# Performance work log

Hardware: AMD Instinct MI355X
Metric: run time of the kernel (lower is better)

## Reference

```python
import jax, jax.numpy as jnp
import numpy as np

B, T, H, W = 64, 14, 96, 96
OUT = 96 * 4  # torchvision Resize(img_size[2]*4) -> 384x384 (input is square)


def _demosaic(img):
    """img: [B, 4, H, W] Bayer planes (rggb) -> [B, 3, 2H, 2W] RGB."""
    b, _, h, w = img.shape
    dt = img.dtype
    # strided scatter of Bayer samples into the 3-channel mosaic grid
    out = jnp.zeros((b, 3, 2 * h, 2 * w), dt)
    out = out.at[:, 0, 0::2, 0::2].set(img[:, 0])  # R
    out = out.at[:, 1, 0::2, 1::2].set(img[:, 1])  # G1
    out = out.at[:, 1, 1::2, 0::2].set(img[:, 2])  # G2
    out = out.at[:, 2, 1::2, 1::2].set(img[:, 3])  # B
    # denominator mask (batch-independent, broadcast over B)
    den = jnp.zeros((1, 3, 2 * h, 2 * w), dt)
    den = den.at[:, 0, 0::2, 0::2].set(1.0)
    den = den.at[:, 1, 0::2, 1::2].set(1.0)
    den = den.at[:, 1, 1::2, 0::2].set(1.0)
    den = den.at[:, 2, 1::2, 1::2].set(1.0)
    # filter_rb = [0.5,1,0.5]^T @ [0.5,1,0.5]; filter_g = plus-shaped
    f_rb = jnp.array([[0.25, 0.5, 0.25], [0.5, 1.0, 0.5], [0.25, 0.5, 0.25]], dt)
    f_g = jnp.array([[0.0, 0.5, 0.0], [0.5, 1.0, 0.5], [0.0, 0.5, 0.0]], dt)
    kern = jnp.stack([f_rb, f_g, f_rb])[:, None]  # [3,1,3,3] depthwise

    def conv(x):
        return jax.lax.conv_general_dilated(
            x, kern, window_strides=(1, 1), padding='SAME',
            dimension_numbers=('NCHW', 'OIHW', 'NCHW'), feature_group_count=3)

    return conv(out) / conv(den)


def setup_inputs() -> dict:
    key = jax.random.key(0)
    frames_batch = jax.random.uniform(key, (B, T, 4, H, W), dtype=jnp.float32)
    return {"frames_batch": frames_batch}


def reference(frames_batch):
    img = frames_batch[:, 0]                      # [B, 4, H, W]
    rgb = _demosaic(img)                          # [B, 3, 2H, 2W]
    # torchvision Resize(384), bilinear, half-pixel centers (upsampling -> no antialias)
    return jax.image.resize(rgb, (rgb.shape[0], 3, OUT, OUT), method='bilinear')
```

## Files before the change

### kernel.cpp

```cpp
#include <hip/hip_runtime.h>

constexpr int Hh = 96, Wh = 96;
constexpr int PLANE = Hh * Wh;
constexpr int BSTRIDE = 14 * 4 * PLANE;
constexpr int DN = 192;
constexpr int ON = 384;
constexpr int QN = 96;
constexpr int KTN = 48;

__device__ __forceinline__ float rcpn(float n) {
  return (n == 2.0f) ? 0.5f : ((n == 3.0f) ? (1.0f / 3.0f) : 0.25f);
}

__device__ __forceinline__ void hblend(float D0, float D1, float D2, float D3,
                                       float* __restrict__ h) {
  h[0] = 0.25f * D0 + 0.75f * D1;
  h[1] = 0.75f * D1 + 0.25f * D2;
  h[2] = 0.25f * D1 + 0.75f * D2;
  h[3] = 0.75f * D2 + 0.25f * D3;
}

template <class F>
__device__ __forceinline__ void stream_rows(F&& rowf, int k0, float* __restrict__ op) {
  float h0[4], h1[4], h2[4];
  rowf((k0 > 0) ? k0 - 1 : 0, h0);
  rowf(k0, h1);
#pragma unroll
  for (int m = 0; m < 4; ++m) {
    const int k = k0 + m;
    float4 v;
    v.x = 0.25f * h0[0] + 0.75f * h1[0];
    v.y = 0.25f * h0[1] + 0.75f * h1[1];
    v.z = 0.25f * h0[2] + 0.75f * h1[2];
    v.w = 0.25f * h0[3] + 0.75f * h1[3];
    *reinterpret_cast<float4*>(op) = v;
    op += ON;
    rowf((k < DN - 1) ? k + 1 : DN - 1, h2);
    v.x = 0.75f * h1[0] + 0.25f * h2[0];
    v.y = 0.75f * h1[1] + 0.25f * h2[1];
    v.z = 0.75f * h1[2] + 0.25f * h2[2];
    v.w = 0.75f * h1[3] + 0.25f * h2[3];
    *reinterpret_cast<float4*>(op) = v;
    op += ON;
#pragma unroll
    for (int j = 0; j < 4; ++j) { h0[j] = h1[j]; h1[j] = h2[j]; }
  }
}

__global__ __launch_bounds__(256) void fused_demosaic_resize(
    const float* __restrict__ in, float* __restrict__ out) {
  const int idx = blockIdx.x * 256 + threadIdx.x;
  const int q = idx % QN;
  int t = idx / QN;
  const int kt = t % KTN; t /= KTN;
  const int ch = t % 3;
  const int b = t / 3;
  const int k0 = kt * 4;

  const int qm = (q > 0) ? q - 1 : 0;
  const int qp = (q < Wh - 1) ? q + 1 : Wh - 1;
  const bool qlo = (q == 0), qhi = (q == Wh - 1);

  const float* base = in + (size_t)b * BSTRIDE;
  float* op = out + (size_t)(((b * 3 + ch) * ON + 2 * k0) * ON + 4 * q);

  if (ch == 0) {
    const float* P = base;
    auto rowf = [&](int r, float* __restrict__ h) {
      const int hr = r >> 1;
      const float* r0 = P + hr * Wh;
      float a = r0[qm], bb = r0[q], c = r0[qp];
      if (r & 1) {
        const float* r1 = P + ((hr < Hh - 1) ? hr + 1 : hr) * Wh;
        a = 0.5f * (a + r1[qm]);
        bb = 0.5f * (bb + r1[q]);
        c = 0.5f * (c + r1[qp]);
      }
      hblend(0.5f * (a + bb), bb, 0.5f * (bb + c), c, h);
    };
    stream_rows(rowf, k0, op);
  } else if (ch == 2) {
    const float* P = base + 3 * PLANE;
    auto rowf = [&](int r, float* __restrict__ h) {
      const int hr = r >> 1;
      const float* r0 = P + hr * Wh;
      float a = r0[qm], bb = r0[q], c = r0[qp];
      if (!(r & 1)) {
        const float* rm = P + ((hr > 0) ? hr - 1 : 0) * Wh;
        a = 0.5f * (a + rm[qm]);
        bb = 0.5f * (bb + rm[q]);
        c = 0.5f * (c + rm[qp]);
      }
      hblend(a, 0.5f * (a + bb), bb, 0.5f * (bb + c), h);
    };
    stream_rows(rowf, k0, op);
  } else {
    const float* G1 = base + PLANE;
    const float* G2 = base + 2 * PLANE;
    const float wQm = qlo ? 0.0f : 1.0f;
    const float wQp = qhi ? 0.0f : 1.0f;
    auto rowf = [&](int r, float* __restrict__ h) {
      const int hr = r >> 1;
      float D0, D1, D2, D3;
      if (r & 1) {
        const float* g1 = G1 + hr * Wh;
        const float* g1p = G1 + ((hr < Hh - 1) ? hr + 1 : hr) * Wh;
        const float* g2 = G2 + hr * Wh;
        const float wD = (hr < Hh - 1) ? 1.0f : 0.0f;
        const float g2qm = g2[qm], g2q = g2[q], g2qp = g2[qp];
        D0 = (g1[qm] + g2qm + g2q + wD * g1p[qm]) * rcpn(3.0f + wD);
        D1 = g2q;
        D2 = (g1[q] + g2q + wD * g1p[q] + wQp * g2qp) * rcpn(2.0f + wD + wQp);
        D3 = g2qp;
      } else {
        const float* g1 = G1 + hr * Wh;
        const float* g2 = G2 + hr * Wh;
        const float* g2m = G2 + ((hr > 0) ? hr - 1 : 0) * Wh;
        const float wU = (hr > 0) ? 1.0f : 0.0f;
        const float g1qm = g1[qm], g1q = g1[q], g1qp = g1[qp];
        D0 = g1qm;
        D1 = (g1q + g2[q] + wQm * g1qm + wU * g2m[q]) * rcpn(2.0f + wQm + wU);
        D2 = g1q;
        D3 = (g1qp + g2[qp] + g1q + wU * g2m[qp]) * rcpn(3.0f + wU);
      }
      if (qlo) D0 = D1;
      if (qhi) D3 = D2;
      hblend(D0, D1, D2, D3, h);
    };
    stream_rows(rowf, k0, op);
  }
}

extern "C" void kernel_launch(void* const* d_in, const int* in_sizes, int n_in,
                              void* d_out, int out_size, void* d_ws, size_t ws_size,
                              hipStream_t stream) {
  const float* in = (const float*)d_in[0];
  float* out = (float*)d_out;
  const int total = 64 * 3 * KTN * QN;
  fused_demosaic_resize<<<total / 256, 256, 0, stream>>>(in, out);
}
```

Before: 25.90 us.

## Preload four half-res rows once per thread and use nontemporal output stores

Each thread now loads the four Bayer-plane rows it needs (3 taps each) up front into registers and derives all six demosaiced rows from them. Before, the rowf lambda re-read overlapping rows for each of the six streamed rows. The six rows are blended into the eight output rows, with edge clamping now handled through the row index list and explicit kt==0 and kt==KTN-1 fixups. Output writes switch to nontemporal vector stores so the large write-only result does not pollute the cache. Register use goes up, and the boundary handling has to match the old per-row clamping exactly.

```diff
diff --git a/kernel.cpp b/kernel.cpp
--- a/kernel.cpp
+++ b/kernel.cpp
@@ -3,10 +3,11 @@
 constexpr int Hh = 96, Wh = 96;
 constexpr int PLANE = Hh * Wh;
 constexpr int BSTRIDE = 14 * 4 * PLANE;
-constexpr int DN = 192;
 constexpr int ON = 384;
 constexpr int QN = 96;
 constexpr int KTN = 48;
+
+typedef float f32x4 __attribute__((ext_vector_type(4)));
 
 __device__ __forceinline__ float rcpn(float n) {
   return (n == 2.0f) ? 0.5f : ((n == 3.0f) ? (1.0f / 3.0f) : 0.25f);
@@ -20,33 +21,6 @@
   h[3] = 0.75f * D2 + 0.25f * D3;
 }
 
-template <class F>
-__device__ __forceinline__ void stream_rows(F&& rowf, int k0, float* __restrict__ op) {
-  float h0[4], h1[4], h2[4];
-  rowf((k0 > 0) ? k0 - 1 : 0, h0);
-  rowf(k0, h1);
-#pragma unroll
-  for (int m = 0; m < 4; ++m) {
-    const int k = k0 + m;
-    float4 v;
-    v.x = 0.25f * h0[0] + 0.75f * h1[0];
-    v.y = 0.25f * h0[1] + 0.75f * h1[1];
-    v.z = 0.25f * h0[2] + 0.75f * h1[2];
-    v.w = 0.25f * h0[3] + 0.75f * h1[3];
-    *reinterpret_cast<float4*>(op) = v;
-    op += ON;
-    rowf((k < DN - 1) ? k + 1 : DN - 1, h2);
-    v.x = 0.75f * h1[0] + 0.25f * h2[0];
-    v.y = 0.75f * h1[1] + 0.25f * h2[1];
-    v.z = 0.75f * h1[2] + 0.25f * h2[2];
-    v.w = 0.75f * h1[3] + 0.25f * h2[3];
-    *reinterpret_cast<float4*>(op) = v;
-    op += ON;
-#pragma unroll
-    for (int j = 0; j < 4; ++j) { h0[j] = h1[j]; h1[j] = h2[j]; }
-  }
-}
-
 __global__ __launch_bounds__(256) void fused_demosaic_resize(
     const float* __restrict__ in, float* __restrict__ out) {
   const int idx = blockIdx.x * 256 + threadIdx.x;
@@ -55,79 +29,110 @@
   const int kt = t % KTN; t /= KTN;
   const int ch = t % 3;
   const int b = t / 3;
-  const int k0 = kt * 4;
 
   const int qm = (q > 0) ? q - 1 : 0;
   const int qp = (q < Wh - 1) ? q + 1 : Wh - 1;
   const bool qlo = (q == 0), qhi = (q == Wh - 1);
 
+  const int pr[4] = { (kt > 0) ? 2 * kt - 1 : 0, 2 * kt, 2 * kt + 1,
+                      (kt < KTN - 1) ? 2 * kt + 2 : Hh - 1 };
+
   const float* base = in + (size_t)b * BSTRIDE;
-  float* op = out + (size_t)(((b * 3 + ch) * ON + 2 * k0) * ON + 4 * q);
 
-  if (ch == 0) {
-    const float* P = base;
-    auto rowf = [&](int r, float* __restrict__ h) {
-      const int hr = r >> 1;
-      const float* r0 = P + hr * Wh;
-      float a = r0[qm], bb = r0[q], c = r0[qp];
-      if (r & 1) {
-        const float* r1 = P + ((hr < Hh - 1) ? hr + 1 : hr) * Wh;
-        a = 0.5f * (a + r1[qm]);
-        bb = 0.5f * (bb + r1[q]);
-        c = 0.5f * (c + r1[qp]);
-      }
-      hblend(0.5f * (a + bb), bb, 0.5f * (bb + c), c, h);
-    };
-    stream_rows(rowf, k0, op);
-  } else if (ch == 2) {
-    const float* P = base + 3 * PLANE;
-    auto rowf = [&](int r, float* __restrict__ h) {
-      const int hr = r >> 1;
-      const float* r0 = P + hr * Wh;
-      float a = r0[qm], bb = r0[q], c = r0[qp];
-      if (!(r & 1)) {
-        const float* rm = P + ((hr > 0) ? hr - 1 : 0) * Wh;
-        a = 0.5f * (a + rm[qm]);
-        bb = 0.5f * (bb + rm[q]);
-        c = 0.5f * (c + rm[qp]);
-      }
-      hblend(a, 0.5f * (a + bb), bb, 0.5f * (bb + c), h);
-    };
-    stream_rows(rowf, k0, op);
-  } else {
+  float h[6][4];
+
+  if (ch == 1) {
     const float* G1 = base + PLANE;
     const float* G2 = base + 2 * PLANE;
+    float g1v[4][3], g2v[4][3];
+#pragma unroll
+    for (int i = 0; i < 4; ++i) {
+      const float* a = G1 + pr[i] * Wh;
+      const float* c = G2 + pr[i] * Wh;
+      g1v[i][0] = a[qm]; g1v[i][1] = a[q]; g1v[i][2] = a[qp];
+      g2v[i][0] = c[qm]; g2v[i][1] = c[q]; g2v[i][2] = c[qp];
+    }
     const float wQm = qlo ? 0.0f : 1.0f;
     const float wQp = qhi ? 0.0f : 1.0f;
-    auto rowf = [&](int r, float* __restrict__ h) {
-      const int hr = r >> 1;
-      float D0, D1, D2, D3;
-      if (r & 1) {
-        const float* g1 = G1 + hr * Wh;
-        const float* g1p = G1 + ((hr < Hh - 1) ? hr + 1 : hr) * Wh;
-        const float* g2 = G2 + hr * Wh;
-        const float wD = (hr < Hh - 1) ? 1.0f : 0.0f;
-        const float g2qm = g2[qm], g2q = g2[q], g2qp = g2[qp];
-        D0 = (g1[qm] + g2qm + g2q + wD * g1p[qm]) * rcpn(3.0f + wD);
-        D1 = g2q;
-        D2 = (g1[q] + g2q + wD * g1p[q] + wQp * g2qp) * rcpn(2.0f + wD + wQp);
-        D3 = g2qp;
-      } else {
-        const float* g1 = G1 + hr * Wh;
-        const float* g2 = G2 + hr * Wh;
-        const float* g2m = G2 + ((hr > 0) ? hr - 1 : 0) * Wh;
-        const float wU = (hr > 0) ? 1.0f : 0.0f;
-        const float g1qm = g1[qm], g1q = g1[q], g1qp = g1[qp];
-        D0 = g1qm;
-        D1 = (g1q + g2[q] + wQm * g1qm + wU * g2m[q]) * rcpn(2.0f + wQm + wU);
-        D2 = g1q;
-        D3 = (g1qp + g2[qp] + g1q + wU * g2m[qp]) * rcpn(3.0f + wU);
-      }
+    auto godd = [&](const float* g1u, const float* g1d, const float* g2,
+                    float wD, float* hh) {
+      float D0 = (g1u[0] + g2[0] + g2[1] + wD * g1d[0]) * rcpn(3.0f + wD);
+      float D1 = g2[1];
+      float D2 = (g1u[1] + g2[1] + wD * g1d[1] + wQp * g2[2]) * rcpn(2.0f + wD + wQp);
+      float D3 = g2[2];
       if (qlo) D0 = D1;
       if (qhi) D3 = D2;
-      hblend(D0, D1, D2, D3, h);
+      hblend(D0, D1, D2, D3, hh);
     };
-    stream_rows(rowf, k0, op);
+    auto geven = [&](const float* g1, const float* g2u, const float* g2d,
+                     float wU, float* hh) {
+      float D0 = g1[0];
+      float D1 = (g1[1] + g2d[1] + wQm * g1[0] + wU * g2u[1]) * rcpn(2.0f + wQm + wU);
+      float D2 = g1[1];
+      float D3 = (g1[2] + g2d[2] + g1[1] + wU * g2u[2]) * rcpn(3.0f + wU);
+      if (qlo) D0 = D1;
+      if (qhi) D3 = D2;
+      hblend(D0, D1, D2, D3, hh);
+    };
+    godd (g1v[0], g1v[1], g2v[0], 1.0f, h[0]);
+    geven(g1v[1], g2v[0], g2v[1], (kt > 0) ? 1.0f : 0.0f, h[1]);
+    godd (g1v[1], g1v[2], g2v[1], 1.0f, h[2]);
+    geven(g1v[2], g2v[1], g2v[2], 1.0f, h[3]);
+    godd (g1v[2], g1v[3], g2v[2], (kt < KTN - 1) ? 1.0f : 0.0f, h[4]);
+    geven(g1v[3], g2v[2], g2v[3], 1.0f, h[5]);
+  } else {
+    const float* P = (ch == 0) ? base : base + 3 * PLANE;
+    float A[4][3];
+#pragma unroll
+    for (int i = 0; i < 4; ++i) {
+      const float* r = P + pr[i] * Wh;
+      A[i][0] = r[qm]; A[i][1] = r[q]; A[i][2] = r[qp];
+    }
+    if (ch == 0) {
+      auto rrow = [&](float a, float b_, float c, float* hh) {
+        hblend(0.5f * (a + b_), b_, 0.5f * (b_ + c), c, hh);
+      };
+      rrow(0.5f * (A[0][0] + A[1][0]), 0.5f * (A[0][1] + A[1][1]), 0.5f * (A[0][2] + A[1][2]), h[0]);
+      rrow(A[1][0], A[1][1], A[1][2], h[1]);
+      rrow(0.5f * (A[1][0] + A[2][0]), 0.5f * (A[1][1] + A[2][1]), 0.5f * (A[1][2] + A[2][2]), h[2]);
+      rrow(A[2][0], A[2][1], A[2][2], h[3]);
+      rrow(0.5f * (A[2][0] + A[3][0]), 0.5f * (A[2][1] + A[3][1]), 0.5f * (A[2][2] + A[3][2]), h[4]);
+      rrow(A[3][0], A[3][1], A[3][2], h[5]);
+    } else {
+      auto brow = [&](float a, float b_, float c, float* hh) {
+        hblend(a, 0.5f * (a + b_), b_, 0.5f * (b_ + c), hh);
+      };
+      brow(A[0][0], A[0][1], A[0][2], h[0]);
+      brow(0.5f * (A[0][0] + A[1][0]), 0.5f * (A[0][1] + A[1][1]), 0.5f * (A[0][2] + A[1][2]), h[1]);
+      brow(A[1][0], A[1][1], A[1][2], h[2]);
+      brow(0.5f * (A[1][0] + A[2][0]), 0.5f * (A[1][1] + A[2][1]), 0.5f * (A[1][2] + A[2][2]), h[3]);
+      brow(A[2][0], A[2][1], A[2][2], h[4]);
+      brow(0.5f * (A[2][0] + A[3][0]), 0.5f * (A[2][1] + A[3][1]), 0.5f * (A[2][2] + A[3][2]), h[5]);
+    }
+  }
+
+#pragma unroll
+  for (int j = 0; j < 4; ++j) {
+    if (kt == 0)       h[0][j] = h[1][j];
+    if (kt == KTN - 1) h[5][j] = h[4][j];
+  }
+
+  float* op = out + (size_t)(((b * 3 + ch) * ON + 8 * kt) * ON + 4 * q);
+#pragma unroll
+  for (int m = 0; m < 4; ++m) {
+    f32x4 v;
+    v.x = 0.25f * h[m][0] + 0.75f * h[m + 1][0];
+    v.y = 0.25f * h[m][1] + 0.75f * h[m + 1][1];
+    v.z = 0.25f * h[m][2] + 0.75f * h[m + 1][2];
+    v.w = 0.25f * h[m][3] + 0.75f * h[m + 1][3];
+    __builtin_nontemporal_store(v, reinterpret_cast<f32x4*>(op));
+    op += ON;
+    v.x = 0.75f * h[m + 1][0] + 0.25f * h[m + 2][0];
+    v.y = 0.75f * h[m + 1][1] + 0.25f * h[m + 2][1];
+    v.z = 0.75f * h[m + 1][2] + 0.25f * h[m + 2][2];
+    v.w = 0.75f * h[m + 1][3] + 0.25f * h[m + 2][3];
+    __builtin_nontemporal_store(v, reinterpret_cast<f32x4*>(op));
+    op += ON;
   }
 }
 
```

Result: faster. 25.08 us (-3.2%).
